# Kernel tuning notes

Hardware: AMD Instinct MI355X
Metric: run time of the kernel (lower is better)

Reference implementation:

```python
import jax, jax.numpy as jnp
import numpy as np

BIG = 1e8  # sentinel 'infinite' squared distance (sqrt(BIG) >> max real distance)


def _edt_sq(feat):
    """Exact squared Euclidean distance transform to the nearest True pixel.
    feat: (H, W) bool. Separable 1-D min-plus envelopes (exact, matches
    scipy.ndimage.distance_transform_edt with unit sampling)."""
    H, W = feat.shape
    f = jnp.where(feat, 0.0, BIG).astype(jnp.float32)
    iw = jnp.arange(W, dtype=jnp.float32)
    sqw = (iw[:, None] - iw[None, :]) ** 2                      # (Wx, Wy)
    d1 = jnp.min(f[:, None, :] + sqw[None, :, :], axis=-1)      # (H, W) row pass
    ih = jnp.arange(H, dtype=jnp.float32)
    sqh = (ih[:, None] - ih[None, :]) ** 2                      # (Hx, Hy)
    d2 = jnp.min(d1[None, :, :] + sqh[:, :, None], axis=1)      # (H, W) col pass
    return d2


def _phi_one(mask):
    # pos: distance to nearest mask==1 pixel (scipy edt of 1-mask)
    # neg: distance to nearest mask==0 pixel (scipy edt of mask)
    pos = jnp.sqrt(_edt_sq(mask))
    neg = jnp.sqrt(_edt_sq(~mask))
    s = mask.sum()
    return jnp.where(s == 0, pos,
                     jnp.where(s == mask.size, -neg, pos - neg + 1.0))


def _boundary_loss(logits, targets):
    B, C, H, W = logits.shape
    probs = jax.nn.softmax(logits, axis=1)
    # one-hot scatter: (B,H,W) -> (B,C,H,W)
    oh = jax.nn.one_hot(targets, C, dtype=jnp.float32).transpose(0, 3, 1, 2)
    masks = (oh > 0.5).reshape(B * C, H, W)
    phi = jax.lax.map(_phi_one, masks).reshape(B, C, H, W)
    phi = jax.lax.stop_gradient(phi)  # torch computes phi under no_grad
    return jnp.mean(probs * phi)


def setup_inputs() -> dict:
    key = jax.random.key(0)
    k1, k2 = jax.random.split(key)
    B, C, H, W = 8, 4, 384, 384
    logits = jax.random.normal(k1, (B, C, H, W), dtype=jnp.float32)
    targets = jax.random.randint(k2, (B, H, W), 0, C, dtype=jnp.int32)
    return {"logits": logits, "targets": targets}


def reference(logits, targets):
    return _boundary_loss(logits, targets)
```

## Files before the change

### kernel.cpp

```cpp
#include <hip/hip_runtime.h>


#define BB 8
#define CC 4
#define HH 384
#define WW 384
#define HW (HH * WW)
#define NTOT 4718592.0f

__global__ __launch_bounds__(384) void k_rowedt(const int* __restrict__ targets,
                                                unsigned short* __restrict__ edt16,
                                                float* __restrict__ out) {
    const int blk = blockIdx.x;
    const int b = blk / HH;
    const int i = blk - b * HH;
    const int j = threadIdx.x;
    const int wv = j >> 6, ln = j & 63;

    __shared__ unsigned long long msk[CC][6];
    const int tj = targets[((size_t)b * HH + i) * WW + j];

    #pragma unroll
    for (int c = 0; c < CC; ++c) {
        const unsigned long long m = __ballot(tj == c);
        if (ln == 0) msk[c][wv] = m;
    }
    __syncthreads();

    #pragma unroll
    for (int c = 0; c < CC; ++c) {
        const unsigned long long w = msk[c][wv];
        int dR = 0xFFFF;
        const unsigned long long x = (ln == 63) ? 0ull : (w >> (ln + 1));
        if (x) {
            dR = __builtin_ctzll(x) + 1;
        } else {
            for (int k = wv + 1; k < 6; ++k) {
                const unsigned long long wk = msk[c][k];
                if (wk) { dR = 64 * k + __builtin_ctzll(wk) - j; break; }
            }
        }
        int dL = 0xFFFF;
        const unsigned long long y = (ln == 0) ? 0ull : (w << (64 - ln));
        if (y) {
            dL = __builtin_clzll(y) + 1;
        } else {
            for (int k = wv - 1; k >= 0; --k) {
                const unsigned long long wk = msk[c][k];
                if (wk) { dL = j - (64 * k + 63 - __builtin_clzll(wk)); break; }
            }
        }
        const int fd = (tj == c) ? 0 : (dR < dL ? dR : dL);
        edt16[(size_t)(b * CC + c) * HW + (size_t)i * WW + j] = (unsigned short)fd;
    }

    if (blk == 0 && j == 0) out[0] = 0.0f;
}

__global__ __launch_bounds__(384) void k_fused(const unsigned short* __restrict__ edt16,
                                               const float* __restrict__ logits,
                                               float* __restrict__ out) {
    const int blk = blockIdx.x;
    const int b = blk / 24;
    const int tile = blk - b * 24;
    const int j0 = tile * 16;
    const int col = threadIdx.x & 15;
    const int rg  = threadIdx.x >> 4;

    __shared__ unsigned short dls[CC][HH][17];

    #pragma unroll
    for (int c = 0; c < CC; ++c) {
        #pragma unroll
        for (int k = 0; k < 16; ++k) {
            const int i = rg + 24 * k;
            dls[c][i][col] =
                edt16[(size_t)(b * CC + c) * HW + (size_t)i * WW + j0 + col];
        }
    }
    __syncthreads();

    float acc = 0.0f;
    #pragma unroll 1
    for (int k = 0; k < 16; ++k) {
        const int i = rg + 24 * k;
        float r4[CC];
        #pragma unroll
        for (int c = 0; c < CC; ++c) {
            const unsigned int v0 = dls[c][i][col];
            float best = (float)(v0 * v0);
            float dd = 1.0f, odd = 3.0f;
            int lo = i, hi = i;
            while (dd < best) {
                lo = (lo > 0) ? lo - 1 : 0;
                hi = (hi < HH - 1) ? hi + 1 : HH - 1;
                const unsigned int a = dls[c][lo][col];
                const unsigned int e = dls[c][hi][col];
                best = fminf(best, fminf((float)(a * a) + dd, (float)(e * e) + dd));
                dd += odd; odd += 2.0f;
            }
            r4[c] = sqrtf(best);
        }
        const float p0 = r4[0] - fminf(r4[1], fminf(r4[2], r4[3])) + 1.0f;
        const float p1 = r4[1] - fminf(r4[0], fminf(r4[2], r4[3])) + 1.0f;
        const float p2 = r4[2] - fminf(r4[0], fminf(r4[1], r4[3])) + 1.0f;
        const float p3 = r4[3] - fminf(r4[0], fminf(r4[1], r4[2])) + 1.0f;

        const size_t po = (size_t)i * WW + j0 + col;
        const size_t pb = (size_t)b * CC * HW;
        const float l0 = logits[pb + 0 * HW + po];
        const float l1 = logits[pb + 1 * HW + po];
        const float l2 = logits[pb + 2 * HW + po];
        const float l3 = logits[pb + 3 * HW + po];
        const float m  = fmaxf(fmaxf(l0, l1), fmaxf(l2, l3));
        const float e0 = __expf(l0 - m), e1 = __expf(l1 - m);
        const float e2 = __expf(l2 - m), e3 = __expf(l3 - m);
        const float inv = 1.0f / (e0 + e1 + e2 + e3);
        acc += inv * (e0 * p0 + e1 * p1 + e2 * p2 + e3 * p3);
    }

    #pragma unroll
    for (int off = 32; off > 0; off >>= 1) acc += __shfl_down(acc, off, 64);
    __shared__ float wsum[6];
    const int wid = threadIdx.x >> 6, ln = threadIdx.x & 63;
    if (ln == 0) wsum[wid] = acc;
    __syncthreads();
    if (threadIdx.x == 0) {
        float tot = 0.0f;
        #pragma unroll
        for (int w = 0; w < 6; ++w) tot += wsum[w];
        atomicAdd(out, tot * (1.0f / NTOT));
    }
}

extern "C" void kernel_launch(void* const* d_in, const int* in_sizes, int n_in,
                              void* d_out, int out_size, void* d_ws, size_t ws_size,
                              hipStream_t stream) {
    const float* logits  = (const float*)d_in[0];
    const int*   targets = (const int*)d_in[1];
    float* out = (float*)d_out;
    unsigned short* edt16 = (unsigned short*)d_ws;

    hipLaunchKernelGGL(k_rowedt, dim3(BB * HH), dim3(WW), 0, stream, targets, edt16, out);
    hipLaunchKernelGGL(k_fused,  dim3(BB * 24), dim3(384), 0, stream, edt16, logits, out);
}
```

Baseline: 103.4 us.

## Narrow column tiles to 12, store squared floats, process channels in two phases

The column-pass kernel now uses 12-column tiles, giving 256 blocks instead of 192 to fill more compute units. It stores precomputed squared distances as floats in shared memory and handles two channels at a time, reusing the buffer between phases. This removes per-iteration int-multiply and convert work from the min-plus search loop and keeps the float shared buffer near the old footprint. In exchange it adds an extra barrier and reload phase, uses modulo-12 thread indexing, and keeps 24 per-thread values live, which may raise register pressure.

```diff
diff --git a/kernel.cpp b/kernel.cpp
--- a/kernel.cpp
+++ b/kernel.cpp
@@ -57,54 +57,78 @@
     if (blk == 0 && j == 0) out[0] = 0.0f;
 }
 
+__device__ __forceinline__ float minplus_col(const float* __restrict__ sqc,
+                                             int i, int col) {
+    float best = sqc[i * 13 + col];
+    float dd = 1.0f, odd = 3.0f;
+    int lo = i, hi = i;
+    while (dd < best) {
+        lo = (lo > 0) ? lo - 1 : 0;
+        hi = (hi < HH - 1) ? hi + 1 : HH - 1;
+        best = fminf(best, fminf(sqc[lo * 13 + col] + dd, sqc[hi * 13 + col] + dd));
+        dd += odd; odd += 2.0f;
+    }
+    return best;
+}
+
 __global__ __launch_bounds__(384) void k_fused(const unsigned short* __restrict__ edt16,
                                                const float* __restrict__ logits,
                                                float* __restrict__ out) {
     const int blk = blockIdx.x;
-    const int b = blk / 24;
-    const int tile = blk - b * 24;
-    const int j0 = tile * 16;
-    const int col = threadIdx.x & 15;
-    const int rg  = threadIdx.x >> 4;
+    const int b = blk >> 5;
+    const int tile = blk & 31;
+    const int j0 = tile * 12;
+    const int col = threadIdx.x % 12;
+    const int rg  = threadIdx.x / 12;
 
-    __shared__ unsigned short dls[CC][HH][17];
+    __shared__ float sq[2][HH][13];
 
     #pragma unroll
-    for (int c = 0; c < CC; ++c) {
+    for (int cc = 0; cc < 2; ++cc) {
         #pragma unroll
-        for (int k = 0; k < 16; ++k) {
-            const int i = rg + 24 * k;
-            dls[c][i][col] =
-                edt16[(size_t)(b * CC + c) * HW + (size_t)i * WW + j0 + col];
+        for (int k = 0; k < 12; ++k) {
+            const int i = rg + 32 * k;
+            const unsigned int v =
+                edt16[(size_t)(b * CC + cc) * HW + (size_t)i * WW + j0 + col];
+            sq[cc][i][col] = (float)(v * v);
+        }
+    }
+    __syncthreads();
+
+    float r01[2][12];
+    #pragma unroll
+    for (int k = 0; k < 12; ++k) {
+        const int i = rg + 32 * k;
+        r01[0][k] = sqrtf(minplus_col(&sq[0][0][0], i, col));
+        r01[1][k] = sqrtf(minplus_col(&sq[1][0][0], i, col));
+    }
+    __syncthreads();
+
+    #pragma unroll
+    for (int cc = 0; cc < 2; ++cc) {
+        #pragma unroll
+        for (int k = 0; k < 12; ++k) {
+            const int i = rg + 32 * k;
+            const unsigned int v =
+                edt16[(size_t)(b * CC + 2 + cc) * HW + (size_t)i * WW + j0 + col];
+            sq[cc][i][col] = (float)(v * v);
         }
     }
     __syncthreads();
 
     float acc = 0.0f;
-    #pragma unroll 1
-    for (int k = 0; k < 16; ++k) {
-        const int i = rg + 24 * k;
-        float r4[CC];
-        #pragma unroll
-        for (int c = 0; c < CC; ++c) {
-            const unsigned int v0 = dls[c][i][col];
-            float best = (float)(v0 * v0);
-            float dd = 1.0f, odd = 3.0f;
-            int lo = i, hi = i;
-            while (dd < best) {
-                lo = (lo > 0) ? lo - 1 : 0;
-                hi = (hi < HH - 1) ? hi + 1 : HH - 1;
-                const unsigned int a = dls[c][lo][col];
-                const unsigned int e = dls[c][hi][col];
-                best = fminf(best, fminf((float)(a * a) + dd, (float)(e * e) + dd));
-                dd += odd; odd += 2.0f;
-            }
-            r4[c] = sqrtf(best);
-        }
-        const float p0 = r4[0] - fminf(r4[1], fminf(r4[2], r4[3])) + 1.0f;
-        const float p1 = r4[1] - fminf(r4[0], fminf(r4[2], r4[3])) + 1.0f;
-        const float p2 = r4[2] - fminf(r4[0], fminf(r4[1], r4[3])) + 1.0f;
-        const float p3 = r4[3] - fminf(r4[0], fminf(r4[1], r4[2])) + 1.0f;
+    #pragma unroll
+    for (int k = 0; k < 12; ++k) {
+        const int i = rg + 32 * k;
+        const float r0 = r01[0][k];
+        const float r1 = r01[1][k];
+        const float r2 = sqrtf(minplus_col(&sq[0][0][0], i, col));
+        const float r3 = sqrtf(minplus_col(&sq[1][0][0], i, col));
+
+        const float p0 = r0 - fminf(r1, fminf(r2, r3)) + 1.0f;
+        const float p1 = r1 - fminf(r0, fminf(r2, r3)) + 1.0f;
+        const float p2 = r2 - fminf(r0, fminf(r1, r3)) + 1.0f;
+        const float p3 = r3 - fminf(r0, fminf(r1, r2)) + 1.0f;
 
         const size_t po = (size_t)i * WW + j0 + col;
         const size_t pb = (size_t)b * CC * HW;
@@ -142,5 +166,5 @@
     unsigned short* edt16 = (unsigned short*)d_ws;
 
     hipLaunchKernelGGL(k_rowedt, dim3(BB * HH), dim3(WW), 0, stream, targets, edt16, out);
-    hipLaunchKernelGGL(k_fused,  dim3(BB * 24), dim3(384), 0, stream, edt16, logits, out);
+    hipLaunchKernelGGL(k_fused,  dim3(BB * 32), dim3(384), 0, stream, edt16, logits, out);
 }
```

Result: no change. 102.1 us (-1.3%).
